# Kernel optimization log

Hardware: AMD Instinct MI355X
Metric: run time of the kernel (lower is better)

The kernel has to match this reference:

```python
import jax, jax.numpy as jnp
import numpy as np

N_NODES = 50000
N_EDGES = 500000
HEADS = 6
CH = 64  # num_hidden == out_dim == 64
IN_DIM = 131
NEG_SLOPE = 0.2


def _gat_conv(h, src, dst, W, a_src, a_dst, b, concat):
    """PyG-style GATConv, add_self_loops=False.
    h: [N, F_in], W: [F_in, H*C], a_src/a_dst: [H, C], b: [H*C] or [C].
    """
    N = h.shape[0]
    x = (h @ W).reshape(N, HEADS, CH)                  # [N,H,C]
    al_s = jnp.sum(x * a_src, axis=-1)                 # [N,H]
    al_d = jnp.sum(x * a_dst, axis=-1)                 # [N,H]
    e = jax.nn.leaky_relu(al_s[src] + al_d[dst], NEG_SLOPE)  # [E,H]
    # segment softmax over destination nodes
    m = jax.ops.segment_max(e, dst, num_segments=N)    # [N,H]
    m = jnp.where(jnp.isfinite(m), m, 0.0)             # isolated nodes -> -inf
    ex = jnp.exp(e - m[dst])                           # [E,H]
    denom = jax.ops.segment_sum(ex, dst, num_segments=N)  # [N,H]
    alpha = ex / (denom[dst] + 1e-16)                  # [E,H]
    out = jax.ops.segment_sum(alpha[:, :, None] * x[src], dst, num_segments=N)  # [N,H,C]
    if concat:
        return out.reshape(N, HEADS * CH) + b
    return out.mean(axis=1) + b


def setup_inputs() -> dict:
    key = jax.random.key(0)
    ks = jax.random.split(key, 20)
    x = jax.random.normal(ks[0], (N_NODES, IN_DIM), dtype=jnp.float32)
    edge_index = jax.random.randint(ks[1], (2, N_EDGES), 0, N_NODES, dtype=jnp.int32)
    d = {"x": x, "edge_index": edge_index}
    in_dims = [IN_DIM, HEADS * CH, HEADS * CH, HEADS * CH]
    for i in range(4):
        kW, kA, kB = jax.random.split(ks[2 + i], 3)
        d[f"W{i}"] = jax.random.normal(kW, (in_dims[i], HEADS * CH), dtype=jnp.float32) * 0.1
        d[f"as{i}"] = jax.random.normal(kA, (HEADS, CH), dtype=jnp.float32) * 0.1
        d[f"ad{i}"] = jax.random.normal(kB, (HEADS, CH), dtype=jnp.float32) * 0.1
        d[f"b{i}"] = jnp.zeros((CH,) if i == 3 else (HEADS * CH,), dtype=jnp.float32)
    return d


def reference(x, edge_index, W0, as0, ad0, b0, W1, as1, ad1, b1,
              W2, as2, ad2, b2, W3, as3, ad3, b3):
    src, dst = edge_index[0], edge_index[1]
    h = jax.nn.elu(_gat_conv(x, src, dst, W0, as0, ad0, b0, True))
    h = jax.nn.elu(_gat_conv(h, src, dst, W1, as1, ad1, b1, True))
    h = jax.nn.elu(_gat_conv(h, src, dst, W2, as2, ad2, b2, True))
    return _gat_conv(h, src, dst, W3, as3, ad3, b3, False)  # [N, 64]
```

## Files before the change

kernel.cpp:

```cpp
#include <hip/hip_runtime.h>

#define N_NODES 50000
#define M_PAD 50048
#define N_EDGES 500000
#define HEADS 6
#define CH 64
#define F_HID 384
#define IN_DIM 131
#define K0PAD 160
#define CAP 64
#define NBM 391
#define ATILE3 98304
#define ATILE0 40960
#define BTILE3 98304
#define BTILE0 40960

static inline int cdiv(int a, int b) { return (a + b - 1) / b; }

typedef __attribute__((ext_vector_type(4))) float f32x4;
typedef __attribute__((ext_vector_type(8))) _Float16 f16x8;
typedef __attribute__((ext_vector_type(4))) _Float16 f16x4;

__device__ __forceinline__ void gload16(const void* g, void* lds) {
  __builtin_amdgcn_global_load_lds((const __attribute__((address_space(1))) void*)g,
                                   (__attribute__((address_space(3))) void*)lds, 16, 0, 0);
}

__global__ void count_kernel(const int* __restrict__ ei, int* __restrict__ deg) {
  int e = blockIdx.x * blockDim.x + threadIdx.x;
  if (e < N_EDGES) atomicAdd(&deg[ei[N_EDGES + e]], 1);
}

__global__ void scan_kernel(const int* __restrict__ deg, int* __restrict__ off,
                            int* __restrict__ cur) {
  __shared__ int sdata[256];
  int tid = threadIdx.x;
  int carry = 0;
  if (tid == 0) off[0] = 0;
  for (int base = 0; base < N_NODES; base += 1024) {
    int idx0 = base + tid * 4;
    int v[4]; int s = 0;
#pragma unroll
    for (int j = 0; j < 4; j++) {
      v[j] = (idx0 + j < N_NODES) ? deg[idx0 + j] : 0;
      s += v[j];
    }
    sdata[tid] = s;
    __syncthreads();
    for (int o = 1; o < 256; o <<= 1) {
      int x = (tid >= o) ? sdata[tid - o] : 0;
      __syncthreads();
      sdata[tid] += x;
      __syncthreads();
    }
    int excl = sdata[tid] - s + carry;
    int total = sdata[255];
    int run = excl;
#pragma unroll
    for (int j = 0; j < 4; j++) {
      if (idx0 + j < N_NODES) cur[idx0 + j] = run;
      run += v[j];
      if (idx0 + j < N_NODES) off[idx0 + j + 1] = run;
    }
    carry += total;
    __syncthreads();
  }
}

__global__ void scatter_kernel(const int* __restrict__ ei, int* __restrict__ cursor,
                               int* __restrict__ csr_src) {
  int e = blockIdx.x * blockDim.x + threadIdx.x;
  if (e < N_EDGES) {
    int d = ei[N_EDGES + e];
    int p = atomicAdd(&cursor[d], 1);
    csr_src[p] = ei[e];
  }
}

#define NXITEMS (M_PAD * (K0PAD / 8))
#define NW0ITEMS (F_HID * (K0PAD / 8))
#define NWITEMS (F_HID * (F_HID / 8))
__global__ void convert_all(const float* __restrict__ x, const float* __restrict__ W0,
                            const float* __restrict__ W1, const float* __restrict__ W2,
                            const float* __restrict__ W3, char* __restrict__ Apk,
                            char* __restrict__ Wt0, char* __restrict__ Wt1,
                            char* __restrict__ Wt2, char* __restrict__ Wt3) {
  int t = blockIdx.x * blockDim.x + threadIdx.x;
  if (t < NXITEMS) {
    const int npc = K0PAD / 8;
    int r = t / npc, g = t % npc;
    int kt = g >> 2, kb = g & 3;
    int k0 = kt * 32 + kb * 8;
    f16x8 hv;
#pragma unroll
    for (int j = 0; j < 8; j++) {
      int k = k0 + j;
      float v = (r < N_NODES && k < IN_DIM) ? x[(long)r * IN_DIM + k] : 0.0f;
      hv[j] = (_Float16)v;
    }
    *(f16x8*)(Apk + (size_t)(r >> 7) * ATILE0 + kt * 8192 + kb * 2048 + (r & 127) * 16) = hv;
  } else if (t < NXITEMS + NW0ITEMS) {
    int u = t - NXITEMS;
    const int npc = K0PAD >> 3;
    int n = u / npc, g = u % npc;
    int kt = g >> 2, kb = g & 3;
    int k0 = kt * 32 + kb * 8;
    f16x8 hv;
#pragma unroll
    for (int j = 0; j < 8; j++) {
      int k = k0 + j;
      float v = (k < IN_DIM) ? W0[(long)k * F_HID + n] : 0.0f;
      hv[j] = (_Float16)v;
    }
    *(f16x8*)(Wt0 + (size_t)(n >> 7) * BTILE0 + kt * 8192 + kb * 2048 + (n & 127) * 16) = hv;
  } else if (t < NXITEMS + NW0ITEMS + 3 * NWITEMS) {
    int u = t - NXITEMS - NW0ITEMS;
    int l = u / NWITEMS;
    u -= l * NWITEMS;
    const float* W = l == 0 ? W1 : (l == 1 ? W2 : W3);
    char* Wt = l == 0 ? Wt1 : (l == 1 ? Wt2 : Wt3);
    const int npc = F_HID >> 3;
    int n = u / npc, g = u % npc;
    int kt = g >> 2, kb = g & 3;
    int k0 = kt * 32 + kb * 8;
    f16x8 hv;
#pragma unroll
    for (int j = 0; j < 8; j++) hv[j] = (_Float16)W[(long)(k0 + j) * F_HID + n];
    *(f16x8*)(Wt + (size_t)(n >> 7) * BTILE3 + kt * 8192 + kb * 2048 + (n & 127) * 16) = hv;
  }
}

template <int K>
__global__ __launch_bounds__(256) void gemm_mfma(const char* __restrict__ Ap,
                                                 const char* __restrict__ Bp,
                                                 const float* __restrict__ AS,
                                                 const float* __restrict__ AD,
                                                 float* __restrict__ als,
                                                 float* __restrict__ ald,
                                                 _Float16* __restrict__ O) {
  constexpr int NKT = K / 32;
  __shared__ __align__(16) char smA[8192];
  __shared__ __align__(16) char smB[8192];
  int xcd = blockIdx.x & 7, slot = blockIdx.x >> 3;
  int bn = slot % 3, tt = slot / 3;
  int bm = tt * 8 + xcd;
  if (bm >= NBM) return;
  int row0 = bm * 128, col0 = bn * 128;
  int tid = threadIdx.x, lane = tid & 63, wv = tid >> 6;
  int wy = wv >> 1, wx = wv & 1;

  f32x4 acc[4][4];
#pragma unroll
  for (int i = 0; i < 4; i++)
#pragma unroll
    for (int j = 0; j < 4; j++) acc[i][j] = (f32x4)0.0f;

  const char* Ab = Ap + (size_t)bm * (NKT * 8192);
  const char* Bb = Bp + (size_t)bn * (NKT * 8192);
  int rsel = lane & 15, ksel = lane >> 4;

  for (int kt = 0; kt < NKT; ++kt) {
#pragma unroll
    for (int i = 0; i < 2; ++i) {
      int b = (i * 4 + wv) * 1024;
      gload16(Ab + (size_t)kt * 8192 + b + lane * 16, smA + b);
      gload16(Bb + (size_t)kt * 8192 + b + lane * 16, smB + b);
    }
    __syncthreads();

    f16x8 av[4], bv[4];
#pragma unroll
    for (int mf = 0; mf < 4; ++mf)
      av[mf] = *(const f16x8*)(smA + ksel * 2048 + (wy * 64 + mf * 16 + rsel) * 16);
#pragma unroll
    for (int nf = 0; nf < 4; ++nf)
      bv[nf] = *(const f16x8*)(smB + ksel * 2048 + (wx * 64 + nf * 16 + rsel) * 16);
#pragma unroll
    for (int mf = 0; mf < 4; ++mf)
#pragma unroll
      for (int nf = 0; nf < 4; ++nf)
        acc[mf][nf] = __builtin_amdgcn_mfma_f32_16x16x32_f16(av[mf], bv[nf], acc[mf][nf], 0, 0, 0);
    __syncthreads();
  }

  int cr = (lane >> 4) * 4, cc = lane & 15;
#pragma unroll
  for (int mf = 0; mf < 4; ++mf)
#pragma unroll
    for (int r = 0; r < 4; ++r) {
      int row = row0 + wy * 64 + mf * 16 + cr + r;
      if (row < N_NODES) {
#pragma unroll
        for (int nf = 0; nf < 4; ++nf)
          O[(size_t)row * F_HID + col0 + wx * 64 + nf * 16 + cc] = (_Float16)acc[mf][nf][r];
      }
    }
  int head = bn * 2 + wx;
  float sa[4], da[4];
#pragma unroll
  for (int nf = 0; nf < 4; ++nf) {
    sa[nf] = AS[head * CH + nf * 16 + cc];
    da[nf] = AD[head * CH + nf * 16 + cc];
  }
#pragma unroll
  for (int mf = 0; mf < 4; ++mf)
#pragma unroll
    for (int r = 0; r < 4; ++r) {
      float ps = 0.0f, pd = 0.0f;
#pragma unroll
      for (int nf = 0; nf < 4; ++nf) {
        ps += acc[mf][nf][r] * sa[nf];
        pd += acc[mf][nf][r] * da[nf];
      }
#pragma unroll
      for (int o = 1; o < 16; o <<= 1) {
        ps += __shfl_xor(ps, o);
        pd += __shfl_xor(pd, o);
      }
      int row = row0 + wy * 64 + mf * 16 + cr + r;
      if (cc == 0 && row < N_NODES) {
        als[row * HEADS + head] = ps;
        ald[row * HEADS + head] = pd;
      }
    }
}

typedef __attribute__((ext_vector_type(4))) _Float16 f16x4t;
#define AGG_CORE(FEAT, OFF, CSR, ALS, ALD)                                        \
  int tid = threadIdx.x;                                                          \
  int sub = tid / 96, t96 = tid - sub * 96;                                       \
  int nb = blockIdx.x * 4;                                                        \
  int n = nb + sub;                                                               \
  int c4 = t96 * 4, h = t96 >> 4;                                                 \
  int o_[5];                                                                      \
  _Pragma("unroll")                                                               \
  for (int k = 0; k < 5; ++k) o_[k] = OFF[nb + k];                                \
  int dmax = 0;                                                                   \
  _Pragma("unroll")                                                               \
  for (int k = 0; k < 4; ++k) dmax = max(dmax, o_[k + 1] - o_[k]);                \
  int nch = (dmax + CAP - 1) / CAP; if (nch < 1) nch = 1;                         \
  int s0 = o_[sub], deg = o_[sub + 1] - o_[sub];                                  \
  int pr = tid >> 4, pl = tid & 15;                                               \
  int psub = pr / 6, ph = pr - psub * 6;                                          \
  int ps0 = o_[psub], pdeg = o_[psub + 1] - o_[psub];                             \
  float pad_ = ALD[(nb + psub) * 6 + ph];                                         \
  float m_run = -INFINITY, s_run = 0.0f;                                          \
  float a0 = 0, a1 = 0, a2 = 0, a3 = 0;                                           \
  for (int ch = 0; ch < nch; ++ch) {                                              \
    int base = ch * CAP;                                                          \
    int cl = deg - base; cl = cl < 0 ? 0 : (cl > CAP ? CAP : cl);                 \
    if (t96 < cl) lsrc[sub][t96] = CSR[s0 + base + t96];                          \
    int pcl = pdeg - base; pcl = pcl < 0 ? 0 : (pcl > CAP ? CAP : pcl);           \
    float asc = 1.0f;                                                             \
    if (pcl > 0) {                                                                \
      float mc = -INFINITY;                                                       \
      for (int i = pl; i < pcl; i += 16) {                                        \
        int s = CSR[ps0 + base + i];                                              \
        float e = ALS[s * 6 + ph] + pad_;                                         \
        e = e > 0.0f ? e : 0.2f * e;                                              \
        lew[psub][ph][i] = e;                                                     \
        mc = fmaxf(mc, e);                                                        \
      }                                                                           \
      mc = fmaxf(mc, __shfl_xor(mc, 1));                                          \
      mc = fmaxf(mc, __shfl_xor(mc, 2));                                          \
      mc = fmaxf(mc, __shfl_xor(mc, 4));                                          \
      mc = fmaxf(mc, __shfl_xor(mc, 8));                                          \
      float mn = fmaxf(m_run, mc);                                                \
      asc = (m_run == -INFINITY) ? 0.0f : __expf(m_run - mn);                     \
      float scp = 0.0f;                                                           \
      for (int i = pl; i < pcl; i += 16) {                                        \
        float wv = __expf(lew[psub][ph][i] - mn);                                 \
        lew[psub][ph][i] = wv;                                                    \
        scp += wv;                                                                \
      }                                                                           \
      scp += __shfl_xor(scp, 1);                                                  \
      scp += __shfl_xor(scp, 2);                                                  \
      scp += __shfl_xor(scp, 4);                                                  \
      scp += __shfl_xor(scp, 8);                                                  \
      s_run = s_run * asc + scp;                                                  \
      m_run = mn;                                                                 \
    }                                                                             \
    if (pl == 0) {                                                                \
      lasc[psub][ph] = asc;                                                       \
      if (ch == nch - 1) lrr[psub][ph] = 1.0f / (s_run + 1e-16f);                 \
    }                                                                             \
    __syncthreads();                                                              \
    float cc0 = 0, cc1 = 0, cc2 = 0, cc3 = 0;                                     \
    int i = 0;                                                                    \
    for (; i + 4 <= cl; i += 4) {                                                 \
      int sA = lsrc[sub][i], sB = lsrc[sub][i + 1];                               \
      int sC = lsrc[sub][i + 2], sD = lsrc[sub][i + 3];                           \
      float wA = lew[sub][h][i], wB = lew[sub][h][i + 1];                         \
      float wC = lew[sub][h][i + 2], wD = lew[sub][h][i + 3];                     \
      f16x4t fA = *(const f16x4t*)(FEAT + (size_t)sA * F_HID + c4);               \
      f16x4t fB = *(const f16x4t*)(FEAT + (size_t)sB * F_HID + c4);               \
      f16x4t fC = *(const f16x4t*)(FEAT + (size_t)sC * F_HID + c4);               \
      f16x4t fD = *(const f16x4t*)(FEAT + (size_t)sD * F_HID + c4);               \
      cc0 += wA * (float)fA[0]; cc1 += wA * (float)fA[1];                         \
      cc2 += wA * (float)fA[2]; cc3 += wA * (float)fA[3];                         \
      cc0 += wB * (float)fB[0]; cc1 += wB * (float)fB[1];                         \
      cc2 += wB * (float)fB[2]; cc3 += wB * (float)fB[3];                         \
      cc0 += wC * (float)fC[0]; cc1 += wC * (float)fC[1];                         \
      cc2 += wC * (float)fC[2]; cc3 += wC * (float)fC[3];                         \
      cc0 += wD * (float)fD[0]; cc1 += wD * (float)fD[1];                         \
      cc2 += wD * (float)fD[2]; cc3 += wD * (float)fD[3];                         \
    }                                                                             \
    for (; i < cl; ++i) {                                                         \
      int s = lsrc[sub][i];                                                       \
      float wv = lew[sub][h][i];                                                  \
      f16x4t fv = *(const f16x4t*)(FEAT + (size_t)s * F_HID + c4);                \
      cc0 += wv * (float)fv[0]; cc1 += wv * (float)fv[1];                         \
      cc2 += wv * (float)fv[2]; cc3 += wv * (float)fv[3];                         \
    }                                                                             \
    float asc2 = lasc[sub][h];                                                    \
    a0 = a0 * asc2 + cc0; a1 = a1 * asc2 + cc1;                                   \
    a2 = a2 * asc2 + cc2; a3 = a3 * asc2 + cc3;                                   \
    __syncthreads();                                                              \
  }                                                                               \
  float rr = lrr[sub][h];

__global__ __launch_bounds__(384) void agg_hidden(const _Float16* __restrict__ feat,
                                                  const int* __restrict__ off,
                                                  const int* __restrict__ csr_src,
                                                  const float* __restrict__ al_s,
                                                  const float* __restrict__ al_d,
                                                  const float* __restrict__ bias,
                                                  char* __restrict__ Apk) {
  __shared__ int   lsrc[4][CAP + 1];
  __shared__ float lew[4][6][CAP + 1];
  __shared__ float lasc[4][6];
  __shared__ float lrr[4][6];
  AGG_CORE(feat, off, csr_src, al_s, al_d)
  float v0 = a0 * rr + bias[c4 + 0];
  float v1 = a1 * rr + bias[c4 + 1];
  float v2 = a2 * rr + bias[c4 + 2];
  float v3 = a3 * rr + bias[c4 + 3];
  v0 = v0 > 0.0f ? v0 : (__expf(v0) - 1.0f);
  v1 = v1 > 0.0f ? v1 : (__expf(v1) - 1.0f);
  v2 = v2 > 0.0f ? v2 : (__expf(v2) - 1.0f);
  v3 = v3 > 0.0f ? v3 : (__expf(v3) - 1.0f);
  f16x4 pv;
  pv[0] = (_Float16)v0; pv[1] = (_Float16)v1;
  pv[2] = (_Float16)v2; pv[3] = (_Float16)v3;
  int kt = c4 >> 5, kb = (c4 >> 3) & 3;
  *(f16x4*)(Apk + (size_t)(n >> 7) * ATILE3 + kt * 8192 + kb * 2048 +
            (n & 127) * 16 + (c4 & 7) * 2) = pv;
}

__global__ __launch_bounds__(384) void agg_out(const _Float16* __restrict__ feat,
                                               const int* __restrict__ off,
                                               const int* __restrict__ csr_src,
                                               const float* __restrict__ al_s,
                                               const float* __restrict__ al_d,
                                               const float* __restrict__ b3,
                                               float* __restrict__ out) {
  __shared__ int   lsrc[4][CAP + 1];
  __shared__ float lew[4][6][CAP + 1];
  __shared__ float lasc[4][6];
  __shared__ float lrr[4][6];
  __shared__ float red[4][384];
  AGG_CORE(feat, off, csr_src, al_s, al_d)
  red[sub][c4 + 0] = a0 * rr;
  red[sub][c4 + 1] = a1 * rr;
  red[sub][c4 + 2] = a2 * rr;
  red[sub][c4 + 3] = a3 * rr;
  __syncthreads();
  if (t96 < 16) {
    int c = t96 * 4;
    f32x4 o = (f32x4)0.0f;
#pragma unroll
    for (int hh = 0; hh < HEADS; hh++) {
#pragma unroll
      for (int j = 0; j < 4; j++) o[j] += red[sub][hh * CH + c + j];
    }
#pragma unroll
    for (int j = 0; j < 4; j++) o[j] = o[j] * (1.0f / 6.0f) + b3[c + j];
    *(f32x4*)(out + (size_t)n * CH + c) = o;
  }
}

extern "C" void kernel_launch(void* const* d_in, const int* in_sizes, int n_in,
                              void* d_out, int out_size, void* d_ws, size_t ws_size,
                              hipStream_t stream) {
  const float* x  = (const float*)d_in[0];
  const int*   ei = (const int*)d_in[1];
  const float* W_[4]  = {(const float*)d_in[2], (const float*)d_in[6],
                         (const float*)d_in[10], (const float*)d_in[14]};
  const float* AS_[4] = {(const float*)d_in[3], (const float*)d_in[7],
                         (const float*)d_in[11], (const float*)d_in[15]};
  const float* AD_[4] = {(const float*)d_in[4], (const float*)d_in[8],
                         (const float*)d_in[12], (const float*)d_in[16]};
  const float* B_[4]  = {(const float*)d_in[5], (const float*)d_in[9],
                         (const float*)d_in[13], (const float*)d_in[17]};
  float* out = (float*)d_out;

  char* w = (char*)d_ws;
  _Float16* feat = (_Float16*)w;
  w += (size_t)N_NODES * F_HID * 2;
  char* Apk = w;
  w += (size_t)NBM * ATILE3;
  char* Wt0 = w; w += 3 * (size_t)BTILE0;
  char* Wt1 = w; w += 3 * (size_t)BTILE3;
  char* Wt2 = w; w += 3 * (size_t)BTILE3;
  char* Wt3 = w; w += 3 * (size_t)BTILE3;
  float* als = (float*)w; w += (size_t)N_NODES * HEADS * 4;
  float* ald = (float*)w; w += (size_t)N_NODES * HEADS * 4;
  int* off = (int*)w; w += (N_NODES + 1) * 4;
  int* cur = (int*)w; w += N_NODES * 4;
  int* deg = (int*)w; w += N_NODES * 4;
  int* csr = (int*)w;

  (void)hipMemsetAsync(deg, 0, N_NODES * sizeof(int), stream);
  count_kernel<<<cdiv(N_EDGES, 256), 256, 0, stream>>>(ei, deg);
  scan_kernel<<<1, 256, 0, stream>>>(deg, off, cur);
  scatter_kernel<<<cdiv(N_EDGES, 256), 256, 0, stream>>>(ei, cur, csr);

  convert_all<<<cdiv(NXITEMS + NW0ITEMS + 3 * NWITEMS, 256), 256, 0, stream>>>(
      x, W_[0], W_[1], W_[2], W_[3], Apk, Wt0, Wt1, Wt2, Wt3);

  const int gemm_grid = 8 * cdiv(NBM, 8) * 3;
  const int agg_grid = N_NODES / 4;

  gemm_mfma<K0PAD><<<gemm_grid, 256, 0, stream>>>(Apk, Wt0, AS_[0], AD_[0], als, ald, feat);
  agg_hidden<<<agg_grid, 384, 0, stream>>>(feat, off, csr, als, ald, B_[0], Apk);

  gemm_mfma<F_HID><<<gemm_grid, 256, 0, stream>>>(Apk, Wt1, AS_[1], AD_[1], als, ald, feat);
  agg_hidden<<<agg_grid, 384, 0, stream>>>(feat, off, csr, als, ald, B_[1], Apk);

  gemm_mfma<F_HID><<<gemm_grid, 256, 0, stream>>>(Apk, Wt2, AS_[2], AD_[2], als, ald, feat);
  agg_hidden<<<agg_grid, 384, 0, stream>>>(feat, off, csr, als, ald, B_[2], Apk);

  gemm_mfma<F_HID><<<gemm_grid, 256, 0, stream>>>(Apk, Wt3, AS_[3], AD_[3], als, ald, feat);
  agg_out<<<agg_grid, 384, 0, stream>>>(feat, off, csr, als, ald, B_[3], out);
}
```

Measured before the change: 607.7 us.

## Sort nodes by in-degree so aggregation blocks process similar-degree nodes

Adds a 64-bucket counting sort of nodes by descending in-degree, built with histogram, scan and scatter kernels. Each aggregation block now handles four nodes of similar degree through an indirection array, so sub-groups waste fewer chunk iterations waiting on the block's maximum degree. The cost is three extra small kernels plus indirect loads of offsets and node ids. Output writes also become scattered rather than contiguous, and there is no locality between nodes that share a block.

Result: slower. 975.1 us (+60.5%).

```diff
diff --git a/kernel.cpp b/kernel.cpp
--- a/kernel.cpp
+++ b/kernel.cpp
@@ -74,6 +74,36 @@
     int d = ei[N_EDGES + e];
     int p = atomicAdd(&cursor[d], 1);
     csr_src[p] = ei[e];
+  }
+}
+
+__global__ void bucket_hist(const int* __restrict__ deg, int* __restrict__ hcnt) {
+  int n = blockIdx.x * blockDim.x + threadIdx.x;
+  if (n < N_NODES) {
+    int b = 63 - min(deg[n], 63);
+    atomicAdd(&hcnt[b], 1);
+  }
+}
+
+__global__ void bucket_scan(const int* __restrict__ hcnt, int* __restrict__ hcur) {
+  int t = threadIdx.x;
+  int c = hcnt[t];
+  int v = c;
+#pragma unroll
+  for (int o = 1; o < 64; o <<= 1) {
+    int u = __shfl_up(v, o);
+    if (t >= o) v += u;
+  }
+  hcur[t] = v - c;
+}
+
+__global__ void bucket_scatter(const int* __restrict__ deg, int* __restrict__ hcur,
+                               int* __restrict__ order) {
+  int n = blockIdx.x * blockDim.x + threadIdx.x;
+  if (n < N_NODES) {
+    int b = 63 - min(deg[n], 63);
+    int p = atomicAdd(&hcur[b], 1);
+    order[p] = n;
   }
 }
 
@@ -226,24 +256,25 @@
 }
 
 typedef __attribute__((ext_vector_type(4))) _Float16 f16x4t;
-#define AGG_CORE(FEAT, OFF, CSR, ALS, ALD)                                        \
+#define AGG_CORE(FEAT, OFF, CSR, ALS, ALD, ORD)                                   \
   int tid = threadIdx.x;                                                          \
   int sub = tid / 96, t96 = tid - sub * 96;                                       \
   int nb = blockIdx.x * 4;                                                        \
-  int n = nb + sub;                                                               \
+  int n = ORD[nb + sub];                                                          \
   int c4 = t96 * 4, h = t96 >> 4;                                                 \
-  int o_[5];                                                                      \
-  _Pragma("unroll")                                                               \
-  for (int k = 0; k < 5; ++k) o_[k] = OFF[nb + k];                                \
   int dmax = 0;                                                                   \
   _Pragma("unroll")                                                               \
-  for (int k = 0; k < 4; ++k) dmax = max(dmax, o_[k + 1] - o_[k]);                \
+  for (int k = 0; k < 4; ++k) {                                                   \
+    int nn = ORD[nb + k];                                                         \
+    dmax = max(dmax, OFF[nn + 1] - OFF[nn]);                                      \
+  }                                                                               \
   int nch = (dmax + CAP - 1) / CAP; if (nch < 1) nch = 1;                         \
-  int s0 = o_[sub], deg = o_[sub + 1] - o_[sub];                                  \
+  int s0 = OFF[n], deg = OFF[n + 1] - s0;                                         \
   int pr = tid >> 4, pl = tid & 15;                                               \
   int psub = pr / 6, ph = pr - psub * 6;                                          \
-  int ps0 = o_[psub], pdeg = o_[psub + 1] - o_[psub];                             \
-  float pad_ = ALD[(nb + psub) * 6 + ph];                                         \
+  int pn = ORD[nb + psub];                                                        \
+  int ps0 = OFF[pn], pdeg = OFF[pn + 1] - ps0;                                    \
+  float pad_ = ALD[pn * 6 + ph];                                                  \
   float m_run = -INFINITY, s_run = 0.0f;                                          \
   float a0 = 0, a1 = 0, a2 = 0, a3 = 0;                                           \
   for (int ch = 0; ch < nch; ++ch) {                                              \
@@ -325,12 +356,13 @@
                                                   const float* __restrict__ al_s,
                                                   const float* __restrict__ al_d,
                                                   const float* __restrict__ bias,
+                                                  const int* __restrict__ order,
                                                   char* __restrict__ Apk) {
   __shared__ int   lsrc[4][CAP + 1];
   __shared__ float lew[4][6][CAP + 1];
   __shared__ float lasc[4][6];
   __shared__ float lrr[4][6];
-  AGG_CORE(feat, off, csr_src, al_s, al_d)
+  AGG_CORE(feat, off, csr_src, al_s, al_d, order)
   float v0 = a0 * rr + bias[c4 + 0];
   float v1 = a1 * rr + bias[c4 + 1];
   float v2 = a2 * rr + bias[c4 + 2];
@@ -353,13 +385,14 @@
                                                const float* __restrict__ al_s,
                                                const float* __restrict__ al_d,
                                                const float* __restrict__ b3,
+                                               const int* __restrict__ order,
                                                float* __restrict__ out) {
   __shared__ int   lsrc[4][CAP + 1];
   __shared__ float lew[4][6][CAP + 1];
   __shared__ float lasc[4][6];
   __shared__ float lrr[4][6];
   __shared__ float red[4][384];
-  AGG_CORE(feat, off, csr_src, al_s, al_d)
+  AGG_CORE(feat, off, csr_src, al_s, al_d, order)
   red[sub][c4 + 0] = a0 * rr;
   red[sub][c4 + 1] = a1 * rr;
   red[sub][c4 + 2] = a2 * rr;
@@ -408,12 +441,18 @@
   int* off = (int*)w; w += (N_NODES + 1) * 4;
   int* cur = (int*)w; w += N_NODES * 4;
   int* deg = (int*)w; w += N_NODES * 4;
+  int* hcnt = (int*)w; w += 64 * 4;
+  int* hcur = (int*)w; w += 64 * 4;
+  int* order = (int*)w; w += N_NODES * 4;
   int* csr = (int*)w;
 
-  (void)hipMemsetAsync(deg, 0, N_NODES * sizeof(int), stream);
+  (void)hipMemsetAsync(deg, 0, (N_NODES + 64) * sizeof(int), stream);
   count_kernel<<<cdiv(N_EDGES, 256), 256, 0, stream>>>(ei, deg);
   scan_kernel<<<1, 256, 0, stream>>>(deg, off, cur);
   scatter_kernel<<<cdiv(N_EDGES, 256), 256, 0, stream>>>(ei, cur, csr);
+  bucket_hist<<<cdiv(N_NODES, 256), 256, 0, stream>>>(deg, hcnt);
+  bucket_scan<<<1, 64, 0, stream>>>(hcnt, hcur);
+  bucket_scatter<<<cdiv(N_NODES, 256), 256, 0, stream>>>(deg, hcur, order);
 
   convert_all<<<cdiv(NXITEMS + NW0ITEMS + 3 * NWITEMS, 256), 256, 0, stream>>>(
       x, W_[0], W_[1], W_[2], W_[3], Apk, Wt0, Wt1, Wt2, Wt3);
@@ -422,14 +461,14 @@
   const int agg_grid = N_NODES / 4;
 
   gemm_mfma<K0PAD><<<gemm_grid, 256, 0, stream>>>(Apk, Wt0, AS_[0], AD_[0], als, ald, feat);
-  agg_hidden<<<agg_grid, 384, 0, stream>>>(feat, off, csr, als, ald, B_[0], Apk);
+  agg_hidden<<<agg_grid, 384, 0, stream>>>(feat, off, csr, als, ald, B_[0], order, Apk);
 
   gemm_mfma<F_HID><<<gemm_grid, 256, 0, stream>>>(Apk, Wt1, AS_[1], AD_[1], als, ald, feat);
-  agg_hidden<<<agg_grid, 384, 0, stream>>>(feat, off, csr, als, ald, B_[1], Apk);
+  agg_hidden<<<agg_grid, 384, 0, stream>>>(feat, off, csr, als, ald, B_[1], order, Apk);
 
   gemm_mfma<F_HID><<<gemm_grid, 256, 0, stream>>>(Apk, Wt2, AS_[2], AD_[2], als, ald, feat);
-  agg_hidden<<<agg_grid, 384, 0, stream>>>(feat, off, csr, als, ald, B_[2], Apk);
+  agg_hidden<<<agg_grid, 384, 0, stream>>>(feat, off, csr, als, ald, B_[2], order, Apk);
 
   gemm_mfma<F_HID><<<gemm_grid, 256, 0, stream>>>(Apk, Wt3, AS_[3], AD_[3], als, ald, feat);
-  agg_out<<<agg_grid, 384, 0, stream>>>(feat, off, csr, als, ald, B_[3], out);
-}
+  agg_out<<<agg_grid, 384, 0, stream>>>(feat, off, csr, als, ald, B_[3], order, out);
+}
```
